# Optimization experiments

Hardware: AMD Instinct MI355X
Metric: run time of the kernel (lower is better)

Reference implementation:

```python
import jax, jax.numpy as jnp
import numpy as np

B, C = 2048, 512          # batch, channels
CHG = 16                  # coarse grid side (16x16 -> N=256)
FHG = 16                  # fine grid side (16x16 -> F=256)
N = CHG * CHG             # coarse_span.total
F = FHG * FHG             # fine_total
K = 4                     # top4 sample mode
LOG_F = float(np.log(F))


def _ln(x, g, b, eps=1e-5):
    m = jnp.mean(x, axis=-1, keepdims=True)
    v = jnp.var(x, axis=-1, keepdims=True)
    return (x - m) * jax.lax.rsqrt(v + eps) * g + b


def _mlp3(x, w1, b1, w2, b2, w3, b3):
    # linear_stack: Linear+gelu, Linear+gelu, Linear (dropout=0 / eval)
    h = jax.nn.gelu(x @ w1 + b1)
    h = jax.nn.gelu(h @ w2 + b2)
    return h @ w3 + b3


def setup_inputs() -> dict:
    key = jax.random.key(0)
    ks = jax.random.split(key, 10)
    s = 0.02
    return {
        'x': jax.random.normal(ks[0], (B, C), jnp.float32),
        'in_g': jnp.ones((C,), jnp.float32), 'in_b': jnp.zeros((C,), jnp.float32),
        'nop_w': jax.random.normal(ks[1], (C, 1), jnp.float32) * s,
        'nop_b': jnp.zeros((1,), jnp.float32),
        'c_w1': jax.random.normal(ks[2], (C, C), jnp.float32) * s,
        'c_b1': jnp.zeros((C,), jnp.float32),
        'c_w2': jax.random.normal(ks[3], (C, C), jnp.float32) * s,
        'c_b2': jnp.zeros((C,), jnp.float32),
        'c_w3': jax.random.normal(ks[4], (C, N), jnp.float32) * s,
        'c_b3': jnp.zeros((N,), jnp.float32),
        'emb': jax.random.normal(ks[5], (N, C), jnp.float32),
        'emb_g': jnp.ones((C,), jnp.float32), 'emb_b': jnp.zeros((C,), jnp.float32),
        'f_w1': jax.random.normal(ks[6], (2 * C, C), jnp.float32) * s,
        'f_b1': jnp.zeros((C,), jnp.float32),
        'f_w2': jax.random.normal(ks[7], (C, C), jnp.float32) * s,
        'f_b2': jnp.zeros((C,), jnp.float32),
        'f_w3': jax.random.normal(ks[8], (C, F), jnp.float32) * s,
        'f_b3': jnp.zeros((F,), jnp.float32),
    }


def reference(x, in_g, in_b, nop_w, nop_b, c_w1, c_b1, c_w2, c_b2, c_w3, c_b3,
              emb, emb_g, emb_b, f_w1, f_b1, f_w2, f_b2, f_w3, f_b3):
    xn = _ln(x, in_g, in_b)                                  # (B,C)
    no_op = xn @ nop_w + nop_b                               # (B,1)
    coarse = _mlp3(xn, c_w1, c_b1, c_w2, c_b2, c_w3, c_b3)   # (B,N)
    _, idx = jax.lax.top_k(coarse, K)                        # (B,K) int32
    e = _ln(emb[idx], emb_g, emb_b)                          # (B,K,C)
    fin = jnp.concatenate([jnp.broadcast_to(xn[:, None, :], (B, K, C)), e], axis=-1)
    fine = _mlp3(fin, f_w1, f_b1, f_w2, f_b2, f_w3, f_b3)    # (B,K,F)
    # scatter value: coarse[b,i] - log F + fine + log F - lse(fine) = coarse[b,i] + log_softmax(fine)
    vals = jnp.take_along_axis(coarse, idx, axis=1)[:, :, None] + jax.nn.log_softmax(fine, axis=-1)
    dense = jnp.broadcast_to((coarse - LOG_F)[:, :, None], (B, N, F))
    dense = dense.at[jnp.arange(B)[:, None], idx].set(vals)  # top-k indices are distinct
    # view (B, ch0, ch1, fh0, fh1) -> permute (0,1,3,2,4) -> flatten
    xname = dense.reshape(B, CHG, CHG, FHG, FHG).transpose(0, 1, 3, 2, 4).reshape(B, -1)
    return jnp.concatenate([no_op, xname], axis=-1)          # (B, 1 + N*F)
```

## Files before the change

kernel.cpp:

```cpp
#include <hip/hip_runtime.h>
#include <math.h>

#define BATCH 2048
#define CH 512
#define N_COARSE 256
#define F_FINE 256
#define K_TOP 4
#define OUT_STRIDE 65537

typedef unsigned short ushort_t;
typedef __bf16 bf16x8 __attribute__((ext_vector_type(8)));
typedef float f32x4 __attribute__((ext_vector_type(4)));

__device__ __forceinline__ float gelu_tanh(float x) {
    float x3 = x * x * x;
    float t = tanhf(0.7978845608028654f * (x + 0.044715f * x3));
    return 0.5f * x * (1.0f + t);
}

__device__ __forceinline__ ushort_t f2bf(float f) {
    unsigned u = __float_as_uint(f);
    unsigned r = (u + 0x7FFF + ((u >> 16) & 1)) >> 16;
    return (ushort_t)r;
}
__device__ __forceinline__ float bf2f(ushort_t h) {
    return __uint_as_float(((unsigned)h) << 16);
}

struct Params {
    const float *x, *in_g, *in_b, *nop_w, *nop_b;
    const float *c_w1, *c_b1, *c_w2, *c_b2, *c_w3, *c_b3;
    const float *emb, *emb_g, *emb_b;
    const float *f_w1, *f_b1, *f_w2, *f_b2, *f_w3, *f_b3;
    float *coarse, *fine, *out, *cvals;
    ushort_t *xnsp, *h1sp, *h2sp, *e_bf, *fh1_bf, *fh2_bf;
    ushort_t *wt1, *wt2, *wt3, *cwt1, *cwt2, *cwt3;
    int *idxb;
};

__global__ __launch_bounds__(256) void prep_kernel(Params p) {
    __shared__ float s[32][33];
    int u = blockIdx.x, t = threadIdx.x;
    if (u < 1536) {
        const float* W; ushort_t* Wt; int Kd, Nd, gx, gy; bool split;
        if (u < 512)       { W=p.f_w1; Wt=p.wt1; Kd=1024; Nd=512; gx=u&15; gy=u>>4; split=false; }
        else if (u < 768)  { int v=u-512;  W=p.f_w2; Wt=p.wt2; Kd=512; Nd=512; gx=v&15; gy=v>>4; split=false; }
        else if (u < 896)  { int v=u-768;  W=p.f_w3; Wt=p.wt3; Kd=512; Nd=256; gx=v&7;  gy=v>>3; split=false; }
        else if (u < 1152) { int v=u-896;  W=p.c_w1; Wt=p.cwt1; Kd=512; Nd=512; gx=v&15; gy=v>>4; split=true; }
        else if (u < 1408) { int v=u-1152; W=p.c_w2; Wt=p.cwt2; Kd=512; Nd=512; gx=v&15; gy=v>>4; split=true; }
        else               { int v=u-1408; W=p.c_w3; Wt=p.cwt3; Kd=512; Nd=256; gx=v&7;  gy=v>>3; split=true; }
        int tx = t & 31, ty = t >> 5;
        int n0 = gx * 32, k0 = gy * 32;
        #pragma unroll
        for (int i = 0; i < 4; ++i) {
            int r = ty + i * 8;
            s[r][tx] = W[(size_t)(k0 + r) * Nd + n0 + tx];
        }
        __syncthreads();
        if (!split) {
            #pragma unroll
            for (int i = 0; i < 4; ++i) {
                int r = ty + i * 8;
                Wt[(size_t)(n0 + r) * Kd + k0 + tx] = f2bf(s[tx][r]);
            }
        } else {
            #pragma unroll
            for (int i = 0; i < 4; ++i) {
                int r = ty + i * 8;
                float v = s[tx][r];
                ushort_t h = f2bf(v);
                Wt[(size_t)(n0 + r) * 1024 + k0 + tx] = h;
                Wt[(size_t)(n0 + r) * 1024 + 512 + k0 + tx] = f2bf(v - bf2f(h));
            }
        }
    } else {
        float* red = &s[0][0];
        int row = u - 1536;
        int lane = t & 63, wave = t >> 6;
        const float* xr = p.x + (size_t)row * CH;
        float v0 = xr[t], v1 = xr[t + 256];
        float sm = v0 + v1, ss = v0 * v0 + v1 * v1;
        #pragma unroll
        for (int off = 32; off; off >>= 1) { sm += __shfl_xor(sm, off); ss += __shfl_xor(ss, off); }
        if (lane == 0) { red[wave] = sm; red[4 + wave] = ss; }
        __syncthreads();
        sm = red[0] + red[1] + red[2] + red[3];
        ss = red[4] + red[5] + red[6] + red[7];
        float mean = sm * (1.0f / CH);
        float var = ss * (1.0f / CH) - mean * mean;
        float rsq = rsqrtf(var + 1e-5f);
        float xn0 = (v0 - mean) * rsq * p.in_g[t] + p.in_b[t];
        float xn1 = (v1 - mean) * rsq * p.in_g[t + 256] + p.in_b[t + 256];
        ushort_t* xr2 = p.xnsp + (size_t)row * 1024;
        ushort_t h0 = f2bf(xn0), h1v = f2bf(xn1);
        xr2[t] = h0; xr2[t + 256] = h1v;
        xr2[512 + t] = f2bf(xn0 - bf2f(h0));
        xr2[512 + t + 256] = f2bf(xn1 - bf2f(h1v));
        float d = xn0 * p.nop_w[t] + xn1 * p.nop_w[t + 256];
        #pragma unroll
        for (int off = 32; off; off >>= 1) d += __shfl_xor(d, off);
        __syncthreads();
        if (lane == 0) red[wave] = d;
        __syncthreads();
        if (t == 0) p.out[(size_t)row * OUT_STRIDE] = red[0] + red[1] + red[2] + red[3] + p.nop_b[0];
    }
}

template<int MODE, int MT, int NT, int OUTM>
__global__ __launch_bounds__(256) void mfma_gemm_kernel(
    const ushort_t* __restrict__ A1, const ushort_t* __restrict__ A2,
    const ushort_t* __restrict__ Wt, const float* __restrict__ bias,
    const float* __restrict__ cvals, void* __restrict__ Cout, int Nd, int Ktot)
{
    constexpr int AI = MT / 64, BI = NT / 64;
    constexpr int FI = MT / 32, FJ = NT / 32;
    __shared__ ushort_t As[2][MT * 32];
    __shared__ ushort_t Bs[2][NT * 32];
    __shared__ float mxs[64 * 2];
    __shared__ float ses[64 * 2];
    int t = threadIdx.x;
    int n0 = blockIdx.x * NT, m0 = blockIdx.y * MT;
    int wave = t >> 6, lane = t & 63;
    int wm = (wave & 1) * (MT / 2), wn = (wave >> 1) * (NT / 2);
    int lr = lane & 15, quad = lane >> 4;

    f32x4 acc[FI][FJ] = {};
    float4 aReg[AI], bReg[BI];

    auto loadAB = [&](int k0) {
        int aoff = (MODE == 2) ? ((k0 >= 1024) ? k0 - 512 : (k0 & 511)) : k0;
        int woff = (MODE == 2) ? ((k0 >= 1024) ? k0 - 1024 : k0) : k0;
        #pragma unroll
        for (int i = 0; i < AI; ++i) {
            int c = i * 256 + t, r = c >> 2, q = (c & 3) * 8;
            int gr = m0 + r;
            const ushort_t* ap;
            if (MODE == 1)      ap = (k0 < 512) ? A1 + (size_t)(gr >> 2) * 1024 + k0 + q
                                                : A2 + (size_t)gr * 512 + (k0 - 512) + q;
            else if (MODE == 2) ap = A1 + (size_t)gr * 1024 + aoff + q;
            else                ap = A1 + (size_t)gr * Ktot + k0 + q;
            aReg[i] = *(const float4*)ap;
        }
        #pragma unroll
        for (int i = 0; i < BI; ++i) {
            int c = i * 256 + t, r = c >> 2, q = (c & 3) * 8;
            size_t wstride = (MODE == 2) ? 1024 : (size_t)Ktot;
            bReg[i] = *(const float4*)(Wt + (size_t)(n0 + r) * wstride + woff + q);
        }
    };
    auto storeAB = [&](int p) {
        #pragma unroll
        for (int i = 0; i < AI; ++i) { int c = i * 256 + t; *(float4*)&As[p][c * 8] = aReg[i]; }
        #pragma unroll
        for (int i = 0; i < BI; ++i) { int c = i * 256 + t; *(float4*)&Bs[p][c * 8] = bReg[i]; }
    };

    loadAB(0);
    storeAB(0);
    int steps = Ktot >> 5;
    int p = 0;
    for (int s = 0; s < steps; ++s) {
        __syncthreads();
        if (s + 1 < steps) loadAB((s + 1) * 32);
        bf16x8 af[FI], bfr[FJ];
        #pragma unroll
        for (int i = 0; i < FI; ++i)
            af[i] = *(const bf16x8*)&As[p][(wm + i * 16 + lr) * 32 + quad * 8];
        #pragma unroll
        for (int j = 0; j < FJ; ++j)
            bfr[j] = *(const bf16x8*)&Bs[p][(wn + j * 16 + lr) * 32 + quad * 8];
        #pragma unroll
        for (int i = 0; i < FI; ++i)
            #pragma unroll
            for (int j = 0; j < FJ; ++j)
                acc[i][j] = __builtin_amdgcn_mfma_f32_16x16x32_bf16(af[i], bfr[j], acc[i][j], 0, 0, 0);
        if (s + 1 < steps) storeAB(p ^ 1);
        p ^= 1;
    }

    if (OUTM == 3) {
        float bv[FJ];
        #pragma unroll
        for (int j = 0; j < FJ; ++j) bv[j] = bias[wn + j * 16 + lr];
        int half = wave >> 1;
        float rmx[FI][4];
        #pragma unroll
        for (int i = 0; i < FI; ++i)
            #pragma unroll
            for (int r = 0; r < 4; ++r) {
                float m = -1e30f;
                #pragma unroll
                for (int j = 0; j < FJ; ++j) m = fmaxf(m, acc[i][j][r] + bv[j]);
                #pragma unroll
                for (int mk = 1; mk < 16; mk <<= 1) m = fmaxf(m, __shfl_xor(m, mk));
                if (lr == 0) mxs[(wm + i * 16 + quad * 4 + r) * 2 + half] = m;
            }
        __syncthreads();
        #pragma unroll
        for (int i = 0; i < FI; ++i)
            #pragma unroll
            for (int r = 0; r < 4; ++r) {
                int rl = wm + i * 16 + quad * 4 + r;
                rmx[i][r] = fmaxf(mxs[rl * 2], mxs[rl * 2 + 1]);
            }
        #pragma unroll
        for (int i = 0; i < FI; ++i)
            #pragma unroll
            for (int r = 0; r < 4; ++r) {
                float sv = 0.f;
                #pragma unroll
                for (int j = 0; j < FJ; ++j) sv += expf(acc[i][j][r] + bv[j] - rmx[i][r]);
                #pragma unroll
                for (int mk = 1; mk < 16; mk <<= 1) sv += __shfl_xor(sv, mk);
                if (lr == 0) ses[(wm + i * 16 + quad * 4 + r) * 2 + half] = sv;
            }
        __syncthreads();
        float* outp = (float*)Cout;
        #pragma unroll
        for (int i = 0; i < FI; ++i)
            #pragma unroll
            for (int r = 0; r < 4; ++r) {
                int rl = wm + i * 16 + quad * 4 + r;
                float se = ses[rl * 2] + ses[rl * 2 + 1];
                float addc = cvals[m0 + rl] - rmx[i][r] - logf(se);
                #pragma unroll
                for (int j = 0; j < FJ; ++j)
                    outp[(size_t)(m0 + rl) * Nd + wn + j * 16 + lr] = acc[i][j][r] + bv[j] + addc;
            }
    } else {
        #pragma unroll
        for (int j = 0; j < FJ; ++j) {
            int col = n0 + wn + j * 16 + lr;
            float bvv = bias[col];
            #pragma unroll
            for (int i = 0; i < FI; ++i) {
                #pragma unroll
                for (int r = 0; r < 4; ++r) {
                    int row = m0 + wm + i * 16 + quad * 4 + r;
                    float val = acc[i][j][r] + bvv;
                    if (OUTM == 0) {
                        ((ushort_t*)Cout)[(size_t)row * Nd + col] = f2bf(gelu_tanh(val));
                    } else if (OUTM == 1) {
                        float gv = gelu_tanh(val);
                        ushort_t h = f2bf(gv);
                        ((ushort_t*)Cout)[(size_t)row * 1024 + col] = h;
                        ((ushort_t*)Cout)[(size_t)row * 1024 + 512 + col] = f2bf(gv - bf2f(h));
                    } else {
                        ((float*)Cout)[(size_t)row * Nd + col] = val;
                    }
                }
            }
        }
    }
}

__global__ __launch_bounds__(256) void topk_embln_kernel(Params p) {
    __shared__ int sidx[4];
    int brow = blockIdx.x, t = threadIdx.x;
    int wave = t >> 6, lane = t & 63;
    if (wave == 0) {
        const float* cr = p.coarse + (size_t)brow * N_COARSE;
        float v[4]; int id[4];
        #pragma unroll
        for (int j = 0; j < 4; ++j) { v[j] = cr[lane + 64 * j]; id[j] = lane + 64 * j; }
        #pragma unroll
        for (int r = 0; r < K_TOP; ++r) {
            float bv = v[0]; int bi = id[0];
            #pragma unroll
            for (int j = 1; j < 4; ++j)
                if (v[j] > bv || (v[j] == bv && id[j] < bi)) { bv = v[j]; bi = id[j]; }
            #pragma unroll
            for (int off = 32; off; off >>= 1) {
                float ov = __shfl_xor(bv, off); int oi = __shfl_xor(bi, off);
                if (ov > bv || (ov == bv && oi < bi)) { bv = ov; bi = oi; }
            }
            if ((bi & 63) == lane) v[bi >> 6] = -INFINITY;
            if (lane == 0) {
                sidx[r] = bi;
                p.idxb[brow * K_TOP + r] = bi;
                p.cvals[brow * K_TOP + r] = bv;
            }
        }
    }
    __syncthreads();
    int n = sidx[wave];
    const float* er = p.emb + (size_t)n * CH + lane * 8;
    float4 u0 = *(const float4*)er;
    float4 u1 = *(const float4*)(er + 4);
    float s  = u0.x + u0.y + u0.z + u0.w + u1.x + u1.y + u1.z + u1.w;
    float ss = u0.x * u0.x + u0.y * u0.y + u0.z * u0.z + u0.w * u0.w
             + u1.x * u1.x + u1.y * u1.y + u1.z * u1.z + u1.w * u1.w;
    #pragma unroll
    for (int off = 32; off; off >>= 1) { s += __shfl_xor(s, off); ss += __shfl_xor(ss, off); }
    float mean = s * (1.0f / CH);
    float var = ss * (1.0f / CH) - mean * mean;
    float rsq = rsqrtf(var + 1e-5f);
    float4 g0 = *(const float4*)(p.emb_g + lane * 8), g1 = *(const float4*)(p.emb_g + lane * 8 + 4);
    float4 b0 = *(const float4*)(p.emb_b + lane * 8), b1 = *(const float4*)(p.emb_b + lane * 8 + 4);
    uint4 pk;
    pk.x = (unsigned)f2bf((u0.x - mean) * rsq * g0.x + b0.x) |
           ((unsigned)f2bf((u0.y - mean) * rsq * g0.y + b0.y) << 16);
    pk.y = (unsigned)f2bf((u0.z - mean) * rsq * g0.z + b0.z) |
           ((unsigned)f2bf((u0.w - mean) * rsq * g0.w + b0.w) << 16);
    pk.z = (unsigned)f2bf((u1.x - mean) * rsq * g1.x + b1.x) |
           ((unsigned)f2bf((u1.y - mean) * rsq * g1.y + b1.y) << 16);
    pk.w = (unsigned)f2bf((u1.z - mean) * rsq * g1.z + b1.z) |
           ((unsigned)f2bf((u1.w - mean) * rsq * g1.w + b1.w) << 16);
    *(uint4*)(p.e_bf + (size_t)(brow * K_TOP + wave) * CH + lane * 8) = pk;
}

__global__ __launch_bounds__(256) void scatter_kernel(Params p) {
    const float LOG_F = 5.545177444479562f;
    int b = blockIdx.y, cx = blockIdx.x, t = threadIdx.x;
    int4 ii = *(const int4*)&p.idxb[b * 4];
    size_t rowb = (size_t)b * OUT_STRIDE + 1;
    #pragma unroll
    for (int q = 0; q < 4; ++q) {
        int o = cx * 4096 + q * 1024 + t * 4;
        int c0 = o >> 12, f0 = (o >> 8) & 15, c1 = (o >> 4) & 15, f1 = o & 15;
        int n = c0 * 16 + c1;
        int f = f0 * 16 + f1;
        int k = -1;
        if (n == ii.x) k = 0; else if (n == ii.y) k = 1; else if (n == ii.z) k = 2; else if (n == ii.w) k = 3;
        float r0, r1, r2, r3;
        if (k >= 0) {
            float4 u = *(const float4*)(p.fine + ((size_t)(b * 4 + k)) * F_FINE + f);
            r0 = u.x; r1 = u.y; r2 = u.z; r3 = u.w;
        } else {
            float base = p.coarse[(size_t)b * N_COARSE + n] - LOG_F;
            r0 = r1 = r2 = r3 = base;
        }
        float* op = p.out + rowb + o;
        __builtin_nontemporal_store(r0, op + 0);
        __builtin_nontemporal_store(r1, op + 1);
        __builtin_nontemporal_store(r2, op + 2);
        __builtin_nontemporal_store(r3, op + 3);
    }
}

extern "C" void kernel_launch(void* const* d_in, const int* in_sizes, int n_in,
                              void* d_out, int out_size, void* d_ws, size_t ws_size,
                              hipStream_t stream) {
    Params prm;
    prm.x     = (const float*)d_in[0];
    prm.in_g  = (const float*)d_in[1];
    prm.in_b  = (const float*)d_in[2];
    prm.nop_w = (const float*)d_in[3];
    prm.nop_b = (const float*)d_in[4];
    prm.c_w1  = (const float*)d_in[5];
    prm.c_b1  = (const float*)d_in[6];
    prm.c_w2  = (const float*)d_in[7];
    prm.c_b2  = (const float*)d_in[8];
    prm.c_w3  = (const float*)d_in[9];
    prm.c_b3  = (const float*)d_in[10];
    prm.emb   = (const float*)d_in[11];
    prm.emb_g = (const float*)d_in[12];
    prm.emb_b = (const float*)d_in[13];
    prm.f_w1  = (const float*)d_in[14];
    prm.f_b1  = (const float*)d_in[15];
    prm.f_w2  = (const float*)d_in[16];
    prm.f_b2  = (const float*)d_in[17];
    prm.f_w3  = (const float*)d_in[18];
    prm.f_b3  = (const float*)d_in[19];

    float* ws = (float*)d_ws;
    prm.coarse  = ws;
    prm.fine    = prm.coarse + 524288;
    prm.xnsp    = (ushort_t*)(prm.fine + 2097152);
    prm.h1sp    = prm.xnsp + 2097152;
    prm.h2sp    = prm.h1sp + 2097152;
    prm.e_bf    = prm.h2sp + 2097152;
    prm.fh1_bf  = prm.e_bf + 4194304;
    prm.fh2_bf  = prm.fh1_bf + 4194304;
    prm.wt1     = prm.fh2_bf + 4194304;
    prm.wt2     = prm.wt1 + 524288;
    prm.wt3     = prm.wt2 + 262144;
    prm.cwt1    = prm.wt3 + 131072;
    prm.cwt2    = prm.cwt1 + 524288;
    prm.cwt3    = prm.cwt2 + 524288;
    prm.idxb    = (int*)(prm.cwt3 + 262144);
    prm.cvals   = (float*)(prm.idxb + 8192);
    prm.out     = (float*)d_out;

    prep_kernel<<<3584, 256, 0, stream>>>(prm);
    mfma_gemm_kernel<2, 64, 64, 1><<<dim3(8, 32), 256, 0, stream>>>(
        prm.xnsp, nullptr, prm.cwt1, prm.c_b1, nullptr, prm.h1sp, 512, 1536);
    mfma_gemm_kernel<2, 64, 64, 1><<<dim3(8, 32), 256, 0, stream>>>(
        prm.h1sp, nullptr, prm.cwt2, prm.c_b2, nullptr, prm.h2sp, 512, 1536);
    mfma_gemm_kernel<2, 64, 64, 2><<<dim3(4, 32), 256, 0, stream>>>(
        prm.h2sp, nullptr, prm.cwt3, prm.c_b3, nullptr, prm.coarse, 256, 1536);
    topk_embln_kernel<<<BATCH, 256, 0, stream>>>(prm);
    mfma_gemm_kernel<1, 64, 64, 0><<<dim3(8, 128), 256, 0, stream>>>(
        prm.xnsp, prm.e_bf, prm.wt1, prm.f_b1, nullptr, prm.fh1_bf, 512, 1024);
    mfma_gemm_kernel<0, 64, 64, 0><<<dim3(8, 128), 256, 0, stream>>>(
        prm.fh1_bf, nullptr, prm.wt2, prm.f_b2, nullptr, prm.fh2_bf, 512, 512);
    mfma_gemm_kernel<0, 64, 256, 3><<<dim3(1, 128), 256, 0, stream>>>(
        prm.fh2_bf, nullptr, prm.wt3, prm.f_b3, prm.cvals, prm.fine, 256, 512);
    scatter_kernel<<<dim3(16, BATCH), 256, 0, stream>>>(prm);
}
```

Measured before the change: 731.2 us.

## Precompute xn half of fine GEMM once per row and scatter fine results directly

The first fine-MLP layer is split algebraically: the xn part of the concatenated input is computed once per batch row (B rows instead of B*K) into a float buffer, and the per-sample GEMM covers only the embedding half, adding the precomputed term before GELU. The final log-softmax GEMM now writes straight into the permuted output layout using the top-k indices, so the scatter kernel only writes the dense coarse baseline and runs before the fine path, which overwrites the selected blocks. The fine GEMMs also use 128-row tiles. This removes a full K-fold redundant half of the largest GEMM and the intermediate fine buffer round-trip, at the cost of relying on launch ordering for the overwrite.

```diff
diff --git a/kernel.cpp b/kernel.cpp
--- a/kernel.cpp
+++ b/kernel.cpp
@@ -32,7 +32,7 @@
     const float *c_w1, *c_b1, *c_w2, *c_b2, *c_w3, *c_b3;
     const float *emb, *emb_g, *emb_b;
     const float *f_w1, *f_b1, *f_w2, *f_b2, *f_w3, *f_b3;
-    float *coarse, *fine, *out, *cvals;
+    float *coarse, *xh, *out, *cvals;
     ushort_t *xnsp, *h1sp, *h2sp, *e_bf, *fh1_bf, *fh2_bf;
     ushort_t *wt1, *wt2, *wt3, *cwt1, *cwt2, *cwt3;
     int *idxb;
@@ -108,16 +108,17 @@
 
 template<int MODE, int MT, int NT, int OUTM>
 __global__ __launch_bounds__(256) void mfma_gemm_kernel(
-    const ushort_t* __restrict__ A1, const ushort_t* __restrict__ A2,
+    const ushort_t* __restrict__ A1,
     const ushort_t* __restrict__ Wt, const float* __restrict__ bias,
-    const float* __restrict__ cvals, void* __restrict__ Cout, int Nd, int Ktot)
+    const float* __restrict__ xtra, const int* __restrict__ idxb,
+    void* __restrict__ Cout, int Nd, int Ktot, int astride, int wstride)
 {
     constexpr int AI = MT / 64, BI = NT / 64;
     constexpr int FI = MT / 32, FJ = NT / 32;
     __shared__ ushort_t As[2][MT * 32];
     __shared__ ushort_t Bs[2][NT * 32];
-    __shared__ float mxs[64 * 2];
-    __shared__ float ses[64 * 2];
+    __shared__ float mxs[MT * 2];
+    __shared__ float ses[MT * 2];
     int t = threadIdx.x;
     int n0 = blockIdx.x * NT, m0 = blockIdx.y * MT;
     int wave = t >> 6, lane = t & 63;
@@ -134,18 +135,15 @@
         for (int i = 0; i < AI; ++i) {
             int c = i * 256 + t, r = c >> 2, q = (c & 3) * 8;
             int gr = m0 + r;
-            const ushort_t* ap;
-            if (MODE == 1)      ap = (k0 < 512) ? A1 + (size_t)(gr >> 2) * 1024 + k0 + q
-                                                : A2 + (size_t)gr * 512 + (k0 - 512) + q;
-            else if (MODE == 2) ap = A1 + (size_t)gr * 1024 + aoff + q;
-            else                ap = A1 + (size_t)gr * Ktot + k0 + q;
+            const ushort_t* ap = (MODE == 2) ? A1 + (size_t)gr * 1024 + aoff + q
+                                             : A1 + (size_t)gr * astride + k0 + q;
             aReg[i] = *(const float4*)ap;
         }
         #pragma unroll
         for (int i = 0; i < BI; ++i) {
             int c = i * 256 + t, r = c >> 2, q = (c & 3) * 8;
-            size_t wstride = (MODE == 2) ? 1024 : (size_t)Ktot;
-            bReg[i] = *(const float4*)(Wt + (size_t)(n0 + r) * wstride + woff + q);
+            size_t ws = (MODE == 2) ? 1024 : (size_t)wstride;
+            bReg[i] = *(const float4*)(Wt + (size_t)(n0 + r) * ws + woff + q);
         }
     };
     auto storeAB = [&](int p) {
@@ -178,7 +176,7 @@
         p ^= 1;
     }
 
-    if (OUTM == 3) {
+    if (OUTM == 4) {
         float bv[FJ];
         #pragma unroll
         for (int j = 0; j < FJ; ++j) bv[j] = bias[wn + j * 16 + lr];
@@ -222,16 +220,20 @@
             for (int r = 0; r < 4; ++r) {
                 int rl = wm + i * 16 + quad * 4 + r;
                 float se = ses[rl * 2] + ses[rl * 2 + 1];
-                float addc = cvals[m0 + rl] - rmx[i][r] - logf(se);
+                int m = m0 + rl;
+                float addc = xtra[m] - rmx[i][r] - logf(se);
+                int n = idxb[m];
+                size_t base = (size_t)(m >> 2) * OUT_STRIDE + 1
+                            + (size_t)((n >> 4) * 4096 + (n & 15) * 16);
                 #pragma unroll
                 for (int j = 0; j < FJ; ++j)
-                    outp[(size_t)(m0 + rl) * Nd + wn + j * 16 + lr] = acc[i][j][r] + bv[j] + addc;
+                    outp[base + ((wn >> 4) + j) * 256 + lr] = acc[i][j][r] + bv[j] + addc;
             }
     } else {
         #pragma unroll
         for (int j = 0; j < FJ; ++j) {
             int col = n0 + wn + j * 16 + lr;
-            float bvv = bias[col];
+            float bvv = (OUTM == 5) ? 0.f : bias[col];
             #pragma unroll
             for (int i = 0; i < FI; ++i) {
                 #pragma unroll
@@ -245,8 +247,11 @@
                         ushort_t h = f2bf(gv);
                         ((ushort_t*)Cout)[(size_t)row * 1024 + col] = h;
                         ((ushort_t*)Cout)[(size_t)row * 1024 + 512 + col] = f2bf(gv - bf2f(h));
+                    } else if (OUTM == 2) {
+                        ((float*)Cout)[(size_t)row * Nd + col] = val;
                     } else {
-                        ((float*)Cout)[(size_t)row * Nd + col] = val;
+                        val += xtra[(size_t)(row >> 2) * Nd + col];
+                        ((ushort_t*)Cout)[(size_t)row * Nd + col] = f2bf(gelu_tanh(val));
                     }
                 }
             }
@@ -312,29 +317,18 @@
 __global__ __launch_bounds__(256) void scatter_kernel(Params p) {
     const float LOG_F = 5.545177444479562f;
     int b = blockIdx.y, cx = blockIdx.x, t = threadIdx.x;
-    int4 ii = *(const int4*)&p.idxb[b * 4];
     size_t rowb = (size_t)b * OUT_STRIDE + 1;
+    const float* cr = p.coarse + (size_t)b * N_COARSE;
     #pragma unroll
     for (int q = 0; q < 4; ++q) {
         int o = cx * 4096 + q * 1024 + t * 4;
-        int c0 = o >> 12, f0 = (o >> 8) & 15, c1 = (o >> 4) & 15, f1 = o & 15;
-        int n = c0 * 16 + c1;
-        int f = f0 * 16 + f1;
-        int k = -1;
-        if (n == ii.x) k = 0; else if (n == ii.y) k = 1; else if (n == ii.z) k = 2; else if (n == ii.w) k = 3;
-        float r0, r1, r2, r3;
-        if (k >= 0) {
-            float4 u = *(const float4*)(p.fine + ((size_t)(b * 4 + k)) * F_FINE + f);
-            r0 = u.x; r1 = u.y; r2 = u.z; r3 = u.w;
-        } else {
-            float base = p.coarse[(size_t)b * N_COARSE + n] - LOG_F;
-            r0 = r1 = r2 = r3 = base;
-        }
+        int n = ((o >> 12) << 4) | ((o >> 4) & 15);
+        float base = cr[n] - LOG_F;
         float* op = p.out + rowb + o;
-        __builtin_nontemporal_store(r0, op + 0);
-        __builtin_nontemporal_store(r1, op + 1);
-        __builtin_nontemporal_store(r2, op + 2);
-        __builtin_nontemporal_store(r3, op + 3);
+        __builtin_nontemporal_store(base, op + 0);
+        __builtin_nontemporal_store(base, op + 1);
+        __builtin_nontemporal_store(base, op + 2);
+        __builtin_nontemporal_store(base, op + 3);
     }
 }
 
@@ -365,8 +359,8 @@
 
     float* ws = (float*)d_ws;
     prm.coarse  = ws;
-    prm.fine    = prm.coarse + 524288;
-    prm.xnsp    = (ushort_t*)(prm.fine + 2097152);
+    prm.xh      = prm.coarse + 524288;
+    prm.xnsp    = (ushort_t*)(prm.xh + 2097152);
     prm.h1sp    = prm.xnsp + 2097152;
     prm.h2sp    = prm.h1sp + 2097152;
     prm.e_bf    = prm.h2sp + 2097152;
@@ -383,18 +377,20 @@
     prm.out     = (float*)d_out;
 
     prep_kernel<<<3584, 256, 0, stream>>>(prm);
+    mfma_gemm_kernel<0, 64, 64, 2><<<dim3(8, 32), 256, 0, stream>>>(
+        prm.xnsp, prm.wt1, prm.f_b1, nullptr, nullptr, prm.xh, 512, 512, 1024, 1024);
     mfma_gemm_kernel<2, 64, 64, 1><<<dim3(8, 32), 256, 0, stream>>>(
-        prm.xnsp, nullptr, prm.cwt1, prm.c_b1, nullptr, prm.h1sp, 512, 1536);
+        prm.xnsp, prm.cwt1, prm.c_b1, nullptr, nullptr, prm.h1sp, 512, 1536, 0, 0);
     mfma_gemm_kernel<2, 64, 64, 1><<<dim3(8, 32), 256, 0, stream>>>(
-        prm.h1sp, nullptr, prm.cwt2, prm.c_b2, nullptr, prm.h2sp, 512, 1536);
+        prm.h1sp, prm.cwt2, prm.c_b2, nullptr, nullptr, prm.h2sp, 512, 1536, 0, 0);
     mfma_gemm_kernel<2, 64, 64, 2><<<dim3(4, 32), 256, 0, stream>>>(
-        prm.h2sp, nullptr, prm.cwt3, prm.c_b3, nullptr, prm.coarse, 256, 1536);
+        prm.h2sp, prm.cwt3, prm.c_b3, nullptr, nullptr, prm.coarse, 256, 1536, 0, 0);
+    scatter_kernel<<<dim3(16, BATCH), 256, 0, stream>>>(prm);
     topk_embln_kernel<<<BATCH, 256, 0, stream>>>(prm);
-    mfma_gemm_kernel<1, 64, 64, 0><<<dim3(8, 128), 256, 0, stream>>>(
-        prm.xnsp, prm.e_bf, prm.wt1, prm.f_b1, nullptr, prm.fh1_bf, 512, 1024);
-    mfma_gemm_kernel<0, 64, 64, 0><<<dim3(8, 128), 256, 0, stream>>>(
-        prm.fh1_bf, nullptr, prm.wt2, prm.f_b2, nullptr, prm.fh2_bf, 512, 512);
-    mfma_gemm_kernel<0, 64, 256, 3><<<dim3(1, 128), 256, 0, stream>>>(
-        prm.fh2_bf, nullptr, prm.wt3, prm.f_b3, prm.cvals, prm.fine, 256, 512);
-    scatter_kernel<<<dim3(16, BATCH), 256, 0, stream>>>(prm);
-}
+    mfma_gemm_kernel<0, 128, 64, 5><<<dim3(8, 64), 256, 0, stream>>>(
+        prm.e_bf, prm.wt1 + 512, nullptr, prm.xh, nullptr, prm.fh1_bf, 512, 512, 512, 1024);
+    mfma_gemm_kernel<0, 128, 64, 0><<<dim3(8, 64), 256, 0, stream>>>(
+        prm.fh1_bf, prm.wt2, prm.f_b2, nullptr, nullptr, prm.fh2_bf, 512, 512, 512, 512);
+    mfma_gemm_kernel<0, 64, 256, 4><<<dim3(1, 128), 256, 0, stream>>>(
+        prm.fh2_bf, prm.wt3, prm.f_b3, prm.cvals, prm.idxb, prm.out, 256, 512, 512, 512);
+}
```

Result: slower. 781.6 us (+6.9%).

## Hoist shared xn half of fine layer-1 GEMM out of per-candidate rows

Applied to the files above, without the earlier changes.

The first fine-MLP layer multiplies concat(xn, e) by f_w1. The xn half is identical for all K=4 candidates, so it is now computed once per batch row (2048 rows) into an fp32 buffer that includes the bias. The per-candidate GEMM then covers only the 512-wide embedding half and adds the precomputed partial before GELU. This removes roughly a quarter of the layer-1 FLOPs. The fine layer-1 and layer-2 GEMMs also move to 128-row tiles, which adds a new fp32 intermediate buffer and an extra kernel launch.

```diff
diff --git a/kernel.cpp b/kernel.cpp
--- a/kernel.cpp
+++ b/kernel.cpp
@@ -32,7 +32,7 @@
     const float *c_w1, *c_b1, *c_w2, *c_b2, *c_w3, *c_b3;
     const float *emb, *emb_g, *emb_b;
     const float *f_w1, *f_b1, *f_w2, *f_b2, *f_w3, *f_b3;
-    float *coarse, *fine, *out, *cvals;
+    float *coarse, *fine, *xh, *out, *cvals;
     ushort_t *xnsp, *h1sp, *h2sp, *e_bf, *fh1_bf, *fh2_bf;
     ushort_t *wt1, *wt2, *wt3, *cwt1, *cwt2, *cwt3;
     int *idxb;
@@ -108,16 +108,17 @@
 
 template<int MODE, int MT, int NT, int OUTM>
 __global__ __launch_bounds__(256) void mfma_gemm_kernel(
-    const ushort_t* __restrict__ A1, const ushort_t* __restrict__ A2,
+    const ushort_t* __restrict__ A1,
     const ushort_t* __restrict__ Wt, const float* __restrict__ bias,
-    const float* __restrict__ cvals, void* __restrict__ Cout, int Nd, int Ktot)
+    const float* __restrict__ xtra,
+    void* __restrict__ Cout, int Nd, int Ktot, int astride, int wstride)
 {
     constexpr int AI = MT / 64, BI = NT / 64;
     constexpr int FI = MT / 32, FJ = NT / 32;
     __shared__ ushort_t As[2][MT * 32];
     __shared__ ushort_t Bs[2][NT * 32];
-    __shared__ float mxs[64 * 2];
-    __shared__ float ses[64 * 2];
+    __shared__ float mxs[MT * 2];
+    __shared__ float ses[MT * 2];
     int t = threadIdx.x;
     int n0 = blockIdx.x * NT, m0 = blockIdx.y * MT;
     int wave = t >> 6, lane = t & 63;
@@ -134,18 +135,15 @@
         for (int i = 0; i < AI; ++i) {
             int c = i * 256 + t, r = c >> 2, q = (c & 3) * 8;
             int gr = m0 + r;
-            const ushort_t* ap;
-            if (MODE == 1)      ap = (k0 < 512) ? A1 + (size_t)(gr >> 2) * 1024 + k0 + q
-                                                : A2 + (size_t)gr * 512 + (k0 - 512) + q;
-            else if (MODE == 2) ap = A1 + (size_t)gr * 1024 + aoff + q;
-            else                ap = A1 + (size_t)gr * Ktot + k0 + q;
+            const ushort_t* ap = (MODE == 2) ? A1 + (size_t)gr * 1024 + aoff + q
+                                             : A1 + (size_t)gr * astride + k0 + q;
             aReg[i] = *(const float4*)ap;
         }
         #pragma unroll
         for (int i = 0; i < BI; ++i) {
             int c = i * 256 + t, r = c >> 2, q = (c & 3) * 8;
-            size_t wstride = (MODE == 2) ? 1024 : (size_t)Ktot;
-            bReg[i] = *(const float4*)(Wt + (size_t)(n0 + r) * wstride + woff + q);
+            size_t ws = (MODE == 2) ? 1024 : (size_t)wstride;
+            bReg[i] = *(const float4*)(Wt + (size_t)(n0 + r) * ws + woff + q);
         }
     };
     auto storeAB = [&](int p) {
@@ -222,7 +220,7 @@
             for (int r = 0; r < 4; ++r) {
                 int rl = wm + i * 16 + quad * 4 + r;
                 float se = ses[rl * 2] + ses[rl * 2 + 1];
-                float addc = cvals[m0 + rl] - rmx[i][r] - logf(se);
+                float addc = xtra[m0 + rl] - rmx[i][r] - logf(se);
                 #pragma unroll
                 for (int j = 0; j < FJ; ++j)
                     outp[(size_t)(m0 + rl) * Nd + wn + j * 16 + lr] = acc[i][j][r] + bv[j] + addc;
@@ -231,7 +229,7 @@
         #pragma unroll
         for (int j = 0; j < FJ; ++j) {
             int col = n0 + wn + j * 16 + lr;
-            float bvv = bias[col];
+            float bvv = (OUTM == 5) ? 0.f : bias[col];
             #pragma unroll
             for (int i = 0; i < FI; ++i) {
                 #pragma unroll
@@ -245,8 +243,11 @@
                         ushort_t h = f2bf(gv);
                         ((ushort_t*)Cout)[(size_t)row * 1024 + col] = h;
                         ((ushort_t*)Cout)[(size_t)row * 1024 + 512 + col] = f2bf(gv - bf2f(h));
+                    } else if (OUTM == 2) {
+                        ((float*)Cout)[(size_t)row * Nd + col] = val;
                     } else {
-                        ((float*)Cout)[(size_t)row * Nd + col] = val;
+                        val += xtra[(size_t)(row >> 2) * Nd + col];
+                        ((ushort_t*)Cout)[(size_t)row * Nd + col] = f2bf(gelu_tanh(val));
                     }
                 }
             }
@@ -380,21 +381,24 @@
     prm.cwt3    = prm.cwt2 + 524288;
     prm.idxb    = (int*)(prm.cwt3 + 262144);
     prm.cvals   = (float*)(prm.idxb + 8192);
+    prm.xh      = prm.cvals + 8192;
     prm.out     = (float*)d_out;
 
     prep_kernel<<<3584, 256, 0, stream>>>(prm);
+    mfma_gemm_kernel<0, 64, 64, 2><<<dim3(8, 32), 256, 0, stream>>>(
+        prm.xnsp, prm.wt1, prm.f_b1, nullptr, prm.xh, 512, 512, 1024, 1024);
     mfma_gemm_kernel<2, 64, 64, 1><<<dim3(8, 32), 256, 0, stream>>>(
-        prm.xnsp, nullptr, prm.cwt1, prm.c_b1, nullptr, prm.h1sp, 512, 1536);
+        prm.xnsp, prm.cwt1, prm.c_b1, nullptr, prm.h1sp, 512, 1536, 0, 0);
     mfma_gemm_kernel<2, 64, 64, 1><<<dim3(8, 32), 256, 0, stream>>>(
-        prm.h1sp, nullptr, prm.cwt2, prm.c_b2, nullptr, prm.h2sp, 512, 1536);
+        prm.h1sp, prm.cwt2, prm.c_b2, nullptr, prm.h2sp, 512, 1536, 0, 0);
     mfma_gemm_kernel<2, 64, 64, 2><<<dim3(4, 32), 256, 0, stream>>>(
-        prm.h2sp, nullptr, prm.cwt3, prm.c_b3, nullptr, prm.coarse, 256, 1536);
+        prm.h2sp, prm.cwt3, prm.c_b3, nullptr, prm.coarse, 256, 1536, 0, 0);
     topk_embln_kernel<<<BATCH, 256, 0, stream>>>(prm);
-    mfma_gemm_kernel<1, 64, 64, 0><<<dim3(8, 128), 256, 0, stream>>>(
-        prm.xnsp, prm.e_bf, prm.wt1, prm.f_b1, nullptr, prm.fh1_bf, 512, 1024);
-    mfma_gemm_kernel<0, 64, 64, 0><<<dim3(8, 128), 256, 0, stream>>>(
-        prm.fh1_bf, nullptr, prm.wt2, prm.f_b2, nullptr, prm.fh2_bf, 512, 512);
+    mfma_gemm_kernel<0, 128, 64, 5><<<dim3(8, 64), 256, 0, stream>>>(
+        prm.e_bf, prm.wt1 + 512, nullptr, prm.xh, prm.fh1_bf, 512, 512, 512, 1024);
+    mfma_gemm_kernel<0, 128, 64, 0><<<dim3(8, 64), 256, 0, stream>>>(
+        prm.fh1_bf, prm.wt2, prm.f_b2, nullptr, prm.fh2_bf, 512, 512, 512, 512);
     mfma_gemm_kernel<0, 64, 256, 3><<<dim3(1, 128), 256, 0, stream>>>(
-        prm.fh2_bf, nullptr, prm.wt3, prm.f_b3, prm.cvals, prm.fine, 256, 512);
+        prm.fh2_bf, prm.wt3, prm.f_b3, prm.cvals, prm.fine, 256, 512, 512, 512);
     scatter_kernel<<<dim3(16, BATCH), 256, 0, stream>>>(prm);
 }
```

Result: slower. 756.5 us (+3.5%).
